# Optimization experiments

Measured on AMD Instinct MI355X. Metric: run time of the kernel, lower is better.

The kernel has to match this reference:

```python
import jax, jax.numpy as jnp
import numpy as np

N = 262144
FEAT = 64
D = 128
DEPTH = 2
N_LAYERS = 1
SCALE_FEATURES = 0.5
SCALE_STEPS = (1.0 - SCALE_FEATURES) / DEPTH
LN_EPS = 1e-5
SLOPE = 0.01


def leaky(x):
    return jnp.where(x >= 0, x, SLOPE * x)


def layernorm(x):
    mu = x.mean(-1, keepdims=True)
    var = ((x - mu) ** 2).mean(-1, keepdims=True)
    return (x - mu) / jnp.sqrt(var + LN_EPS)


def setup_inputs() -> dict:
    key = jax.random.key(0)
    ks = jax.random.split(key, 12)
    raw_feats = jax.random.normal(ks[0], (N, FEAT), dtype=jnp.float32)
    uids = jnp.arange(N, dtype=jnp.int32)
    id_map = jax.random.randint(ks[1], (N, 1, 2), 0, N, dtype=jnp.int32)
    # FeatureEmbedder params
    slow_mean = jnp.zeros((FEAT,), jnp.float32)
    slow_std = jnp.ones((FEAT,), jnp.float32)
    W_embd = jax.random.normal(ks[2], (FEAT, D), jnp.float32) / np.sqrt(FEAT)
    b_embd = jnp.zeros((D,), jnp.float32)
    Wl = jax.random.normal(ks[3], (N_LAYERS, D, D), jnp.float32) / np.sqrt(D)
    bl = jnp.zeros((N_LAYERS, D), jnp.float32)
    # node_emb params
    W_node = jax.random.normal(ks[4], (D, D), jnp.float32) / np.sqrt(D)
    b_node = jnp.zeros((D,), jnp.float32)
    rezero = jnp.full((1,), 0.1, jnp.float32)  # nonzero so depth loop is active
    W_w = jax.random.normal(ks[5], (D, 1), jnp.float32) * 0.01
    W_v = jax.random.normal(ks[6], (D, 1), jnp.float32) / np.sqrt(D)
    return {
        'raw_feats': raw_feats, 'uids': uids, 'id_map': id_map,
        'slow_mean': slow_mean, 'slow_std': slow_std,
        'W_embd': W_embd, 'b_embd': b_embd, 'Wl': Wl, 'bl': bl,
        'W_node': W_node, 'b_node': b_node, 'rezero': rezero,
        'W_w': W_w, 'W_v': W_v,
    }


def reference(raw_feats, uids, id_map, slow_mean, slow_std, W_embd, b_embd,
              Wl, bl, W_node, b_node, rezero, W_w, W_v):
    # sorted_feats = cat([raw_feats, zeros(1, FEAT)])  -> [N+1, FEAT]
    sorted_feats = jnp.concatenate(
        [raw_feats, jnp.zeros((1, FEAT), raw_feats.dtype)], axis=0)

    # FeatureEmbedder: SlowNorm -> Linear -> leaky, residual blocks, LayerNorm, *scale
    x = (sorted_feats - slow_mean) / (slow_std + 0.001)
    x = leaky(x @ W_embd + b_embd)
    for i in range(N_LAYERS):
        # F.leaky_relu(Sequential(Linear, LeakyReLU)(x)) + x  (double leaky)
        x = leaky(leaky(x @ Wl[i] + bl[i])) + x
    x = layernorm(x) * SCALE_FEATURES  # [N+1, D]

    # uids == arange(N), so uid-value -> row-index lookup is identity
    ids = id_map[:, 0, :]  # [N, 2] row indices into x

    for _ in range(DEPTH):
        feats = x[ids].mean(axis=1)                 # gather [N,2,D] -> mean -> [N,D]
        feats = leaky(feats @ W_node + b_node)       # node_emb
        new = x[:-1] + feats * (SCALE_STEPS * rezero)
        x = jnp.concatenate([new, x[-1:]], axis=0)   # scatter-update rows [:-1]

    x_main = x[:-1]
    w = x_main @ W_w                                  # weight head, no bias
    v = jax.lax.stop_gradient(x_main) @ W_v           # value head on detached x
    return (x_main, w, v)
```

## Files before the change

### kernel.cpp

```cpp
#include <hip/hip_runtime.h>


#define NROWS 262144
#define NBLK  4096

typedef __attribute__((ext_vector_type(8))) short bhalf8;
typedef __attribute__((ext_vector_type(4))) float f32x4;
typedef __attribute__((ext_vector_type(4))) unsigned int u32x4;

__device__ __forceinline__ unsigned short f2bf(float x) {
    union { float f; unsigned u; } v; v.f = x;
    unsigned r = v.u + 0x7FFFu + ((v.u >> 16) & 1u);
    return (unsigned short)(r >> 16);
}
__device__ __forceinline__ float bflo(unsigned u) {
    union { unsigned u; float f; } v; v.u = u << 16; return v.f;
}
__device__ __forceinline__ float bfhi(unsigned u) {
    union { unsigned u; float f; } v; v.u = u & 0xFFFF0000u; return v.f;
}
__device__ __forceinline__ float leaky(float x) { return x >= 0.0f ? x : 0.01f * x; }

__global__ void __launch_bounds__(256)
setup_kernel(const float* __restrict__ smean, const float* __restrict__ sstd,
             const float* __restrict__ Wemb, const float* __restrict__ bemb,
             const float* __restrict__ Wl, const float* __restrict__ Wn,
             unsigned short* __restrict__ wpack, float* __restrict__ bembP)
{
    int task = blockIdx.x * 256 + threadIdx.x;
    if (blockIdx.x < 160) {
        if (task < 8192) {
            int f = task >> 9, idx = task & 511;
            int t = f >> 1, s = f & 1, lane = idx >> 3, j = idx & 7;
            int n = t * 16 + (lane & 15), k = s * 32 + (lane >> 4) * 8 + j;
            wpack[task] = f2bf(Wemb[k * 128 + n] / (sstd[k] + 0.001f));
        } else if (task < 24576) {
            int u = task - 8192;
            int f = u >> 9, idx = u & 511;
            int t = f >> 2, s = f & 3, lane = idx >> 3, j = idx & 7;
            int n = t * 16 + (lane & 15), k = s * 32 + (lane >> 4) * 8 + j;
            wpack[task] = f2bf(Wl[k * 128 + n]);
        } else if (task < 40960) {
            int u = task - 24576;
            int f = u >> 9, idx = u & 511;
            int t = f >> 2, s = f & 3, lane = idx >> 3, j = idx & 7;
            int n = t * 16 + (lane & 15), k = s * 32 + (lane >> 4) * 8 + j;
            wpack[task] = f2bf(0.5f * Wn[k * 128 + n]);
        }
    } else {
        int n = threadIdx.x;
        if (n < 128) {
            float acc = bemb[n];
            for (int k = 0; k < 64; k++)
                acc -= smean[k] / (sstd[k] + 0.001f) * Wemb[k * 128 + n];
            bembP[n] = acc;
        }
    }
}

__global__ void __launch_bounds__(256)
phase_a_kernel(const float* __restrict__ feats,
               const unsigned short* __restrict__ wembF,
               const float* __restrict__ bembP,
               const unsigned short* __restrict__ wlF,
               const float* __restrict__ bl,
               unsigned short* __restrict__ xout)
{
    __shared__ __align__(16) short hb[64 * 136];
    const int tid = threadIdx.x, lane = tid & 63, wv = tid >> 6;
    const int m = lane & 15, q = lane >> 4;
    const int r0 = blockIdx.x * 64;

    const bhalf8* wbe = (const bhalf8*)wembF;
    const bhalf8* wbl = (const bhalf8*)wlF;

    bhalf8 af[2];
    #pragma unroll
    for (int s = 0; s < 2; s++) {
        const float* fp = feats + (size_t)(r0 + wv * 16 + m) * 64 + s * 32 + q * 8;
        f32x4 f0 = *(const f32x4*)fp;
        f32x4 f1 = *(const f32x4*)(fp + 4);
        bhalf8 a;
        #pragma unroll
        for (int jj = 0; jj < 4; jj++) { a[jj] = (short)f2bf(f0[jj]); a[4 + jj] = (short)f2bf(f1[jj]); }
        af[s] = a;
    }
    f32x4 acc[8] = {};
    #pragma unroll
    for (int s = 0; s < 2; s++)
        #pragma unroll
        for (int t = 0; t < 8; t++)
            acc[t] = __builtin_amdgcn_mfma_f32_16x16x32_bf16(af[s], wbe[(t * 2 + s) * 64 + lane], acc[t], 0, 0, 0);

    float hv[8][4];
    #pragma unroll
    for (int t = 0; t < 8; t++) {
        float be = bembP[t * 16 + m];
        #pragma unroll
        for (int p = 0; p < 4; p++) {
            float h = leaky(acc[t][p] + be);
            hv[t][p] = h;
            hb[(wv * 16 + q * 4 + p) * 136 + t * 16 + m] = (short)f2bf(h);
        }
    }
    f32x4 acc2[8] = {};
    #pragma unroll
    for (int s = 0; s < 4; s++) {
        bhalf8 a = *(const bhalf8*)&hb[(wv * 16 + m) * 136 + s * 32 + q * 8];
        #pragma unroll
        for (int t = 0; t < 8; t++)
            acc2[t] = __builtin_amdgcn_mfma_f32_16x16x32_bf16(a, wbl[(t * 4 + s) * 64 + lane], acc2[t], 0, 0, 0);
    }

    float tv[8][4];
    float sum[4] = {0, 0, 0, 0}, ssq[4] = {0, 0, 0, 0};
    #pragma unroll
    for (int t = 0; t < 8; t++) {
        float bb = bl[t * 16 + m];
        #pragma unroll
        for (int p = 0; p < 4; p++) {
            float v = leaky(leaky(acc2[t][p] + bb)) + hv[t][p];
            tv[t][p] = v;
            sum[p] += v; ssq[p] += v * v;
        }
    }
    #pragma unroll
    for (int p = 0; p < 4; p++) {
        #pragma unroll
        for (int d = 1; d < 16; d <<= 1) {
            sum[p] += __shfl_xor(sum[p], d, 64);
            ssq[p] += __shfl_xor(ssq[p], d, 64);
        }
    }
    #pragma unroll
    for (int p = 0; p < 4; p++) {
        float mu  = sum[p] * (1.0f / 128.0f);
        float var = ssq[p] * (1.0f / 128.0f) - mu * mu;
        float rs  = rsqrtf(var + 1e-5f) * 0.5f;
        int row = wv * 16 + q * 4 + p;
        #pragma unroll
        for (int t = 0; t < 8; t++)
            hb[row * 136 + t * 16 + m] = (short)f2bf((tv[t][p] - mu) * rs);
    }
    __syncthreads();
    for (int c = tid; c < 64 * 16; c += 256) {
        int row = c >> 4, cb = (c & 15) * 8;
        *reinterpret_cast<u32x4*>(&xout[(size_t)(r0 + row) * 128 + cb]) =
            *reinterpret_cast<const u32x4*>(&hb[row * 136 + cb]);
    }
}

template <typename TOUT>
__global__ void __launch_bounds__(256)
prop_kernel(const unsigned short* __restrict__ xin, const int* __restrict__ idmap,
            const unsigned short* __restrict__ wnF, const float* __restrict__ bn,
            const float* __restrict__ rez, const float* __restrict__ Ww,
            const float* __restrict__ Wv, TOUT* __restrict__ xout,
            float* __restrict__ wout, float* __restrict__ vout, int final_pass)
{
    __shared__ __align__(16) short gls[64 * 136];
    const int tid = threadIdx.x, lane = tid & 63, wv = tid >> 6;
    const int m = lane & 15, q = lane >> 4;
    const int r0 = blockIdx.x * 64;
    const bhalf8* wbn = (const bhalf8*)wnF;

    const int myrow = r0 + wv * 16 + m;
    int2 ids = ((const int2*)idmap)[myrow];
    const unsigned short* xa = xin + (size_t)ids.x * 128;
    const unsigned short* xb = xin + (size_t)ids.y * 128;
    bhalf8 afr[4];
    #pragma unroll
    for (int s = 0; s < 4; s++) {
        u32x4 ua = *(const u32x4*)(xa + s * 32 + q * 8);
        u32x4 ub = *(const u32x4*)(xb + s * 32 + q * 8);
        bhalf8 o;
        #pragma unroll
        for (int w = 0; w < 4; w++) {
            float lo = bflo(ua[w]) + bflo(ub[w]);
            float hi = bfhi(ua[w]) + bfhi(ub[w]);
            o[2 * w]     = (short)f2bf(lo);
            o[2 * w + 1] = (short)f2bf(hi);
        }
        afr[s] = o;
    }

    f32x4 acc[8] = {};
    #pragma unroll
    for (int s = 0; s < 4; s++)
        #pragma unroll
        for (int t = 0; t < 8; t++)
            acc[t] = __builtin_amdgcn_mfma_f32_16x16x32_bf16(afr[s], wbn[(t * 4 + s) * 64 + lane], acc[t], 0, 0, 0);

    const float scale = 0.25f * rez[0];
    #pragma unroll
    for (int t = 0; t < 8; t++) {
        float bb = bn[t * 16 + m];
        #pragma unroll
        for (int p = 0; p < 4; p++)
            gls[(wv * 16 + q * 4 + p) * 136 + t * 16 + m] = (short)f2bf(leaky(acc[t][p] + bb) * scale);
    }
    __syncthreads();

    #pragma unroll
    for (int i = 0; i < 4; i++) {
        int task = i * 256 + tid;
        int row = task >> 4, cb = task & 15;
        u32x4 gv = *(const u32x4*)&gls[row * 136 + cb * 8];
        u32x4 xv = *(const u32x4*)(xin + (size_t)(r0 + row) * 128 + cb * 8);
        float xn[8];
        #pragma unroll
        for (int w = 0; w < 4; w++) {
            xn[2 * w]     = bflo(xv[w]) + bflo(gv[w]);
            xn[2 * w + 1] = bfhi(xv[w]) + bfhi(gv[w]);
        }
        if (!final_pass) {
            u32x4 ov;
            #pragma unroll
            for (int w = 0; w < 4; w++)
                ov[w] = (unsigned)f2bf(xn[2 * w]) | ((unsigned)f2bf(xn[2 * w + 1]) << 16);
            *reinterpret_cast<u32x4*>(reinterpret_cast<unsigned short*>(xout) + (size_t)(r0 + row) * 128 + cb * 8) = ov;
        } else {
            float* op = reinterpret_cast<float*>(xout) + (size_t)(r0 + row) * 128 + cb * 8;
            f32x4 o0, o1;
            #pragma unroll
            for (int w = 0; w < 4; w++) { o0[w] = xn[w]; o1[w] = xn[4 + w]; }
            *reinterpret_cast<f32x4*>(op)     = o0;
            *reinterpret_cast<f32x4*>(op + 4) = o1;
            f32x4 w0 = *(const f32x4*)&Ww[cb * 8], w1 = *(const f32x4*)&Ww[cb * 8 + 4];
            f32x4 v0 = *(const f32x4*)&Wv[cb * 8], v1 = *(const f32x4*)&Wv[cb * 8 + 4];
            float ws = 0.0f, vs = 0.0f;
            #pragma unroll
            for (int w = 0; w < 4; w++) {
                ws += xn[w] * w0[w] + xn[4 + w] * w1[w];
                vs += xn[w] * v0[w] + xn[4 + w] * v1[w];
            }
            #pragma unroll
            for (int d = 1; d < 16; d <<= 1) {
                ws += __shfl_xor(ws, d, 64);
                vs += __shfl_xor(vs, d, 64);
            }
            if ((lane & 15) == 0) { wout[r0 + row] = ws; vout[r0 + row] = vs; }
        }
    }
}

extern "C" void kernel_launch(void* const* d_in, const int* in_sizes, int n_in,
                              void* d_out, int out_size, void* d_ws, size_t ws_size,
                              hipStream_t stream) {
    const float* feats = (const float*)d_in[0];
    const int*   idmap = (const int*)d_in[2];
    const float* smean = (const float*)d_in[3];
    const float* sstd  = (const float*)d_in[4];
    const float* Wemb  = (const float*)d_in[5];
    const float* bemb  = (const float*)d_in[6];
    const float* Wl    = (const float*)d_in[7];
    const float* bl    = (const float*)d_in[8];
    const float* Wn    = (const float*)d_in[9];
    const float* bn    = (const float*)d_in[10];
    const float* rez   = (const float*)d_in[11];
    const float* Ww    = (const float*)d_in[12];
    const float* Wv    = (const float*)d_in[13];

    char* ws = (char*)d_ws;
    unsigned short* wpack = (unsigned short*)ws;
    float*          bembP = (float*)(ws + 81920);
    unsigned short* x1    = (unsigned short*)(ws + (1 << 20));

    float* out = (float*)d_out;
    unsigned short* x0 = (unsigned short*)d_out;
    float* wout = out + (size_t)NROWS * 128;
    float* vout = wout + NROWS;

    setup_kernel<<<161, 256, 0, stream>>>(smean, sstd, Wemb, bemb, Wl, Wn, wpack, bembP);
    phase_a_kernel<<<NBLK, 256, 0, stream>>>(feats, wpack, bembP, wpack + 8192, bl, x0);
    prop_kernel<unsigned short><<<NBLK, 256, 0, stream>>>(x0, idmap, wpack + 24576, bn, rez, Ww, Wv,
                                                          x1, nullptr, nullptr, 0);
    prop_kernel<float><<<NBLK, 256, 0, stream>>>(x1, idmap, wpack + 24576, bn, rez, Ww, Wv,
                                                 out, wout, vout, 1);
}
```

Before: 344.8 us.

## Gather neighbor rows from an fp8 shadow copy to halve random-gather traffic

Phase A and the first propagation pass now also write an fp8 copy of x, laid out so each lane's K-slices sit contiguously. The propagation kernels gather the two neighbor rows from this fp8 copy instead of the bf16 copy, cutting the bytes of the random gather in half. The kernel also prefetches its own x rows into registers early and adds occupancy hints to the launch bounds. The cost is extra fp8 writes and a precision loss on the gathered features, which could break tolerance.

```diff
diff --git a/kernel.cpp b/kernel.cpp
--- a/kernel.cpp
+++ b/kernel.cpp
@@ -6,7 +6,9 @@
 
 typedef __attribute__((ext_vector_type(8))) short bhalf8;
 typedef __attribute__((ext_vector_type(4))) float f32x4;
+typedef __attribute__((ext_vector_type(2))) float f32x2;
 typedef __attribute__((ext_vector_type(4))) unsigned int u32x4;
+typedef __attribute__((ext_vector_type(2))) unsigned int u32x2;
 
 __device__ __forceinline__ unsigned short f2bf(float x) {
     union { float f; unsigned u; } v; v.f = x;
@@ -20,6 +22,12 @@
     union { unsigned u; float f; } v; v.u = u & 0xFFFF0000u; return v.f;
 }
 __device__ __forceinline__ float leaky(float x) { return x >= 0.0f ? x : 0.01f * x; }
+
+__device__ __forceinline__ unsigned pk4fp8(float a, float b, float c, float d) {
+    int r = __builtin_amdgcn_cvt_pk_fp8_f32(a, b, 0, false);
+    r = __builtin_amdgcn_cvt_pk_fp8_f32(c, d, r, true);
+    return (unsigned)r;
+}
 
 __global__ void __launch_bounds__(256)
 setup_kernel(const float* __restrict__ smean, const float* __restrict__ sstd,
@@ -58,13 +66,14 @@
     }
 }
 
-__global__ void __launch_bounds__(256)
+__global__ void __launch_bounds__(256, 4)
 phase_a_kernel(const float* __restrict__ feats,
                const unsigned short* __restrict__ wembF,
                const float* __restrict__ bembP,
                const unsigned short* __restrict__ wlF,
                const float* __restrict__ bl,
-               unsigned short* __restrict__ xout)
+               unsigned short* __restrict__ xout,
+               unsigned char* __restrict__ xf8)
 {
     __shared__ __align__(16) short hb[64 * 136];
     const int tid = threadIdx.x, lane = tid & 63, wv = tid >> 6;
@@ -92,16 +101,19 @@
         for (int t = 0; t < 8; t++)
             acc[t] = __builtin_amdgcn_mfma_f32_16x16x32_bf16(af[s], wbe[(t * 2 + s) * 64 + lane], acc[t], 0, 0, 0);
 
-    float hv[8][4];
+    unsigned hvp[8][2];
     #pragma unroll
     for (int t = 0; t < 8; t++) {
         float be = bembP[t * 16 + m];
+        unsigned short hq[4];
         #pragma unroll
         for (int p = 0; p < 4; p++) {
             float h = leaky(acc[t][p] + be);
-            hv[t][p] = h;
-            hb[(wv * 16 + q * 4 + p) * 136 + t * 16 + m] = (short)f2bf(h);
-        }
+            hq[p] = f2bf(h);
+            hb[(wv * 16 + q * 4 + p) * 136 + t * 16 + m] = (short)hq[p];
+        }
+        hvp[t][0] = (unsigned)hq[0] | ((unsigned)hq[1] << 16);
+        hvp[t][1] = (unsigned)hq[2] | ((unsigned)hq[3] << 16);
     }
     f32x4 acc2[8] = {};
     #pragma unroll
@@ -117,9 +129,12 @@
     #pragma unroll
     for (int t = 0; t < 8; t++) {
         float bb = bl[t * 16 + m];
+        float h0 = bflo(hvp[t][0]), h1 = bfhi(hvp[t][0]);
+        float h2 = bflo(hvp[t][1]), h3 = bfhi(hvp[t][1]);
+        float hvv[4] = { h0, h1, h2, h3 };
         #pragma unroll
         for (int p = 0; p < 4; p++) {
-            float v = leaky(leaky(acc2[t][p] + bb)) + hv[t][p];
+            float v = leaky(leaky(acc2[t][p] + bb)) + hvv[p];
             tv[t][p] = v;
             sum[p] += v; ssq[p] += v * v;
         }
@@ -144,18 +159,25 @@
     }
     __syncthreads();
     for (int c = tid; c < 64 * 16; c += 256) {
-        int row = c >> 4, cb = (c & 15) * 8;
-        *reinterpret_cast<u32x4*>(&xout[(size_t)(r0 + row) * 128 + cb]) =
-            *reinterpret_cast<const u32x4*>(&hb[row * 136 + cb]);
+        int row = c >> 4, cb = c & 15;
+        u32x4 hv4 = *reinterpret_cast<const u32x4*>(&hb[row * 136 + cb * 8]);
+        *reinterpret_cast<u32x4*>(&xout[(size_t)(r0 + row) * 128 + cb * 8]) = hv4;
+        u32x2 pf;
+        pf[0] = pk4fp8(bflo(hv4[0]), bfhi(hv4[0]), bflo(hv4[1]), bfhi(hv4[1]));
+        pf[1] = pk4fp8(bflo(hv4[2]), bfhi(hv4[2]), bflo(hv4[3]), bfhi(hv4[3]));
+        *reinterpret_cast<u32x2*>(xf8 + (size_t)(r0 + row) * 128 + (cb & 3) * 32 + (cb >> 2) * 8) = pf;
     }
 }
 
 template <typename TOUT>
-__global__ void __launch_bounds__(256)
-prop_kernel(const unsigned short* __restrict__ xin, const int* __restrict__ idmap,
+__global__ void __launch_bounds__(256, 5)
+prop_kernel(const unsigned short* __restrict__ xin,
+            const unsigned char* __restrict__ xf8,
+            const int* __restrict__ idmap,
             const unsigned short* __restrict__ wnF, const float* __restrict__ bn,
             const float* __restrict__ rez, const float* __restrict__ Ww,
             const float* __restrict__ Wv, TOUT* __restrict__ xout,
+            unsigned char* __restrict__ xf8out,
             float* __restrict__ wout, float* __restrict__ vout, int final_pass)
 {
     __shared__ __align__(16) short gls[64 * 136];
@@ -164,23 +186,41 @@
     const int r0 = blockIdx.x * 64;
     const bhalf8* wbn = (const bhalf8*)wnF;
 
+    const int crow = tid >> 4, ccb = tid & 15;
+    u32x4 xown[4];
+    #pragma unroll
+    for (int i = 0; i < 4; i++)
+        xown[i] = *reinterpret_cast<const u32x4*>(xin + (size_t)(r0 + i * 16 + crow) * 128 + ccb * 8);
+
     const int myrow = r0 + wv * 16 + m;
     int2 ids = ((const int2*)idmap)[myrow];
-    const unsigned short* xa = xin + (size_t)ids.x * 128;
-    const unsigned short* xb = xin + (size_t)ids.y * 128;
+    const unsigned char* pa = xf8 + (size_t)ids.x * 128 + q * 32;
+    const unsigned char* pb = xf8 + (size_t)ids.y * 128 + q * 32;
+    u32x4 ga0 = *(const u32x4*)pa;
+    u32x4 ga1 = *(const u32x4*)(pa + 16);
+    u32x4 gb0 = *(const u32x4*)pb;
+    u32x4 gb1 = *(const u32x4*)(pb + 16);
+
     bhalf8 afr[4];
     #pragma unroll
     for (int s = 0; s < 4; s++) {
-        u32x4 ua = *(const u32x4*)(xa + s * 32 + q * 8);
-        u32x4 ub = *(const u32x4*)(xb + s * 32 + q * 8);
+        unsigned a0 = (s < 2) ? ga0[(s & 1) * 2]     : ga1[(s & 1) * 2];
+        unsigned a1 = (s < 2) ? ga0[(s & 1) * 2 + 1] : ga1[(s & 1) * 2 + 1];
+        unsigned b0 = (s < 2) ? gb0[(s & 1) * 2]     : gb1[(s & 1) * 2];
+        unsigned b1 = (s < 2) ? gb0[(s & 1) * 2 + 1] : gb1[(s & 1) * 2 + 1];
+        f32x2 s01 = __builtin_amdgcn_cvt_pk_f32_fp8((int)a0, false);
+        f32x2 s23 = __builtin_amdgcn_cvt_pk_f32_fp8((int)a0, true);
+        f32x2 s45 = __builtin_amdgcn_cvt_pk_f32_fp8((int)a1, false);
+        f32x2 s67 = __builtin_amdgcn_cvt_pk_f32_fp8((int)a1, true);
+        f32x2 t01 = __builtin_amdgcn_cvt_pk_f32_fp8((int)b0, false);
+        f32x2 t23 = __builtin_amdgcn_cvt_pk_f32_fp8((int)b0, true);
+        f32x2 t45 = __builtin_amdgcn_cvt_pk_f32_fp8((int)b1, false);
+        f32x2 t67 = __builtin_amdgcn_cvt_pk_f32_fp8((int)b1, true);
         bhalf8 o;
-        #pragma unroll
-        for (int w = 0; w < 4; w++) {
-            float lo = bflo(ua[w]) + bflo(ub[w]);
-            float hi = bfhi(ua[w]) + bfhi(ub[w]);
-            o[2 * w]     = (short)f2bf(lo);
-            o[2 * w + 1] = (short)f2bf(hi);
-        }
+        o[0] = (short)f2bf(s01[0] + t01[0]); o[1] = (short)f2bf(s01[1] + t01[1]);
+        o[2] = (short)f2bf(s23[0] + t23[0]); o[3] = (short)f2bf(s23[1] + t23[1]);
+        o[4] = (short)f2bf(s45[0] + t45[0]); o[5] = (short)f2bf(s45[1] + t45[1]);
+        o[6] = (short)f2bf(s67[0] + t67[0]); o[7] = (short)f2bf(s67[1] + t67[1]);
         afr[s] = o;
     }
 
@@ -203,10 +243,9 @@
 
     #pragma unroll
     for (int i = 0; i < 4; i++) {
-        int task = i * 256 + tid;
-        int row = task >> 4, cb = task & 15;
+        int row = i * 16 + crow, cb = ccb;
         u32x4 gv = *(const u32x4*)&gls[row * 136 + cb * 8];
-        u32x4 xv = *(const u32x4*)(xin + (size_t)(r0 + row) * 128 + cb * 8);
+        u32x4 xv = xown[i];
         float xn[8];
         #pragma unroll
         for (int w = 0; w < 4; w++) {
@@ -219,6 +258,10 @@
             for (int w = 0; w < 4; w++)
                 ov[w] = (unsigned)f2bf(xn[2 * w]) | ((unsigned)f2bf(xn[2 * w + 1]) << 16);
             *reinterpret_cast<u32x4*>(reinterpret_cast<unsigned short*>(xout) + (size_t)(r0 + row) * 128 + cb * 8) = ov;
+            u32x2 pf;
+            pf[0] = pk4fp8(xn[0], xn[1], xn[2], xn[3]);
+            pf[1] = pk4fp8(xn[4], xn[5], xn[6], xn[7]);
+            *reinterpret_cast<u32x2*>(xf8out + (size_t)(r0 + row) * 128 + (cb & 3) * 32 + (cb >> 2) * 8) = pf;
         } else {
             float* op = reinterpret_cast<float*>(xout) + (size_t)(r0 + row) * 128 + cb * 8;
             f32x4 o0, o1;
@@ -264,7 +307,9 @@
     char* ws = (char*)d_ws;
     unsigned short* wpack = (unsigned short*)ws;
     float*          bembP = (float*)(ws + 81920);
-    unsigned short* x1    = (unsigned short*)(ws + (1 << 20));
+    unsigned short* x1    = (unsigned short*)(ws + (1ull << 20));
+    unsigned char*  x0f8  = (unsigned char*)(ws + (65ull << 20));
+    unsigned char*  x1f8  = (unsigned char*)(ws + (97ull << 20));
 
     float* out = (float*)d_out;
     unsigned short* x0 = (unsigned short*)d_out;
@@ -272,9 +317,9 @@
     float* vout = wout + NROWS;
 
     setup_kernel<<<161, 256, 0, stream>>>(smean, sstd, Wemb, bemb, Wl, Wn, wpack, bembP);
-    phase_a_kernel<<<NBLK, 256, 0, stream>>>(feats, wpack, bembP, wpack + 8192, bl, x0);
-    prop_kernel<unsigned short><<<NBLK, 256, 0, stream>>>(x0, idmap, wpack + 24576, bn, rez, Ww, Wv,
-                                                          x1, nullptr, nullptr, 0);
-    prop_kernel<float><<<NBLK, 256, 0, stream>>>(x1, idmap, wpack + 24576, bn, rez, Ww, Wv,
-                                                 out, wout, vout, 1);
-}
+    phase_a_kernel<<<NBLK, 256, 0, stream>>>(feats, wpack, bembP, wpack + 8192, bl, x0, x0f8);
+    prop_kernel<unsigned short><<<NBLK, 256, 0, stream>>>(x0, x0f8, idmap, wpack + 24576, bn, rez, Ww, Wv,
+                                                          x1, x1f8, nullptr, nullptr, 0);
+    prop_kernel<float><<<NBLK, 256, 0, stream>>>(x1, x1f8, idmap, wpack + 24576, bn, rez, Ww, Wv,
+                                                 out, nullptr, wout, vout, 1);
+}
```

Measured after the change: 344.3 us. No clear change (-0.2%).

## Make phase_a and prop kernels persistent with register prefetch of next tile

Applied to the files above, without the earlier changes.

Shrinks the grid from 4096 to 1024 blocks; each block now loops over four 64-row tiles and prefetches the next tile's features, id pairs, gathered rows and own rows into registers while the current tile computes. Shared buffers are double-buffered per iteration, and phase_a rereads the residual from LDS instead of keeping it in registers. The aim is to hide gather and load latency behind MFMA work. The cost is more register pressure (launch bounds now request occupancy) and fewer blocks in flight to hide latency.

```diff
diff --git a/kernel.cpp b/kernel.cpp
--- a/kernel.cpp
+++ b/kernel.cpp
@@ -2,7 +2,8 @@
 
 
 #define NROWS 262144
-#define NBLK  4096
+#define NTILES 4096
+#define GRID  1024
 
 typedef __attribute__((ext_vector_type(8))) short bhalf8;
 typedef __attribute__((ext_vector_type(4))) float f32x4;
@@ -18,6 +19,9 @@
 }
 __device__ __forceinline__ float bfhi(unsigned u) {
     union { unsigned u; float f; } v; v.u = u & 0xFFFF0000u; return v.f;
+}
+__device__ __forceinline__ float bf2f(unsigned short s) {
+    union { unsigned u; float f; } v; v.u = ((unsigned)s) << 16; return v.f;
 }
 __device__ __forceinline__ float leaky(float x) { return x >= 0.0f ? x : 0.01f * x; }
 
@@ -58,7 +62,7 @@
     }
 }
 
-__global__ void __launch_bounds__(256)
+__global__ void __launch_bounds__(256, 4)
 phase_a_kernel(const float* __restrict__ feats,
                const unsigned short* __restrict__ wembF,
                const float* __restrict__ bembP,
@@ -66,180 +70,238 @@
                const float* __restrict__ bl,
                unsigned short* __restrict__ xout)
 {
-    __shared__ __align__(16) short hb[64 * 136];
+    __shared__ __align__(16) short hb[2][64 * 136];
     const int tid = threadIdx.x, lane = tid & 63, wv = tid >> 6;
     const int m = lane & 15, q = lane >> 4;
-    const int r0 = blockIdx.x * 64;
+    const int crow = tid >> 4, ccb = tid & 15;
 
     const bhalf8* wbe = (const bhalf8*)wembF;
     const bhalf8* wbl = (const bhalf8*)wlF;
 
-    bhalf8 af[2];
+    f32x4 fr[4], nfr[4];
+    {
+        const float* base = feats + (size_t)(blockIdx.x * 64 + wv * 16 + m) * 64 + q * 8;
+        #pragma unroll
+        for (int s = 0; s < 2; s++) {
+            fr[2 * s]     = *(const f32x4*)(base + s * 32);
+            fr[2 * s + 1] = *(const f32x4*)(base + s * 32 + 4);
+        }
+    }
+
     #pragma unroll
-    for (int s = 0; s < 2; s++) {
-        const float* fp = feats + (size_t)(r0 + wv * 16 + m) * 64 + s * 32 + q * 8;
-        f32x4 f0 = *(const f32x4*)fp;
-        f32x4 f1 = *(const f32x4*)(fp + 4);
-        bhalf8 a;
-        #pragma unroll
-        for (int jj = 0; jj < 4; jj++) { a[jj] = (short)f2bf(f0[jj]); a[4 + jj] = (short)f2bf(f1[jj]); }
-        af[s] = a;
-    }
-    f32x4 acc[8] = {};
-    #pragma unroll
-    for (int s = 0; s < 2; s++)
-        #pragma unroll
-        for (int t = 0; t < 8; t++)
-            acc[t] = __builtin_amdgcn_mfma_f32_16x16x32_bf16(af[s], wbe[(t * 2 + s) * 64 + lane], acc[t], 0, 0, 0);
-
-    float hv[8][4];
-    #pragma unroll
-    for (int t = 0; t < 8; t++) {
-        float be = bembP[t * 16 + m];
+    for (int it = 0; it < 4; ++it) {
+        const int r0 = (blockIdx.x + it * GRID) * 64;
+        if (it < 3) {
+            const float* base = feats + (size_t)(r0 + GRID * 64 + wv * 16 + m) * 64 + q * 8;
+            #pragma unroll
+            for (int s = 0; s < 2; s++) {
+                nfr[2 * s]     = *(const f32x4*)(base + s * 32);
+                nfr[2 * s + 1] = *(const f32x4*)(base + s * 32 + 4);
+            }
+        }
+        short* hbb = hb[it & 1];
+
+        bhalf8 af[2];
+        #pragma unroll
+        for (int s = 0; s < 2; s++) {
+            bhalf8 a;
+            #pragma unroll
+            for (int jj = 0; jj < 4; jj++) {
+                a[jj]     = (short)f2bf(fr[2 * s][jj]);
+                a[4 + jj] = (short)f2bf(fr[2 * s + 1][jj]);
+            }
+            af[s] = a;
+        }
+        f32x4 acc[8] = {};
+        #pragma unroll
+        for (int s = 0; s < 2; s++)
+            #pragma unroll
+            for (int t = 0; t < 8; t++)
+                acc[t] = __builtin_amdgcn_mfma_f32_16x16x32_bf16(af[s], wbe[(t * 2 + s) * 64 + lane], acc[t], 0, 0, 0);
+
+        #pragma unroll
+        for (int t = 0; t < 8; t++) {
+            float be = bembP[t * 16 + m];
+            #pragma unroll
+            for (int p = 0; p < 4; p++)
+                hbb[(wv * 16 + q * 4 + p) * 136 + t * 16 + m] = (short)f2bf(leaky(acc[t][p] + be));
+        }
+        f32x4 acc2[8] = {};
+        #pragma unroll
+        for (int s = 0; s < 4; s++) {
+            bhalf8 a = *(const bhalf8*)&hbb[(wv * 16 + m) * 136 + s * 32 + q * 8];
+            #pragma unroll
+            for (int t = 0; t < 8; t++)
+                acc2[t] = __builtin_amdgcn_mfma_f32_16x16x32_bf16(a, wbl[(t * 4 + s) * 64 + lane], acc2[t], 0, 0, 0);
+        }
+
+        float sum[4] = {0, 0, 0, 0}, ssq[4] = {0, 0, 0, 0};
+        #pragma unroll
+        for (int t = 0; t < 8; t++) {
+            float bb = bl[t * 16 + m];
+            #pragma unroll
+            for (int p = 0; p < 4; p++) {
+                float h = bf2f((unsigned short)hbb[(wv * 16 + q * 4 + p) * 136 + t * 16 + m]);
+                float v = leaky(leaky(acc2[t][p] + bb)) + h;
+                acc2[t][p] = v;
+                sum[p] += v; ssq[p] += v * v;
+            }
+        }
         #pragma unroll
         for (int p = 0; p < 4; p++) {
-            float h = leaky(acc[t][p] + be);
-            hv[t][p] = h;
-            hb[(wv * 16 + q * 4 + p) * 136 + t * 16 + m] = (short)f2bf(h);
-        }
-    }
-    f32x4 acc2[8] = {};
-    #pragma unroll
-    for (int s = 0; s < 4; s++) {
-        bhalf8 a = *(const bhalf8*)&hb[(wv * 16 + m) * 136 + s * 32 + q * 8];
-        #pragma unroll
-        for (int t = 0; t < 8; t++)
-            acc2[t] = __builtin_amdgcn_mfma_f32_16x16x32_bf16(a, wbl[(t * 4 + s) * 64 + lane], acc2[t], 0, 0, 0);
-    }
-
-    float tv[8][4];
-    float sum[4] = {0, 0, 0, 0}, ssq[4] = {0, 0, 0, 0};
-    #pragma unroll
-    for (int t = 0; t < 8; t++) {
-        float bb = bl[t * 16 + m];
+            #pragma unroll
+            for (int d = 1; d < 16; d <<= 1) {
+                sum[p] += __shfl_xor(sum[p], d, 64);
+                ssq[p] += __shfl_xor(ssq[p], d, 64);
+            }
+        }
         #pragma unroll
         for (int p = 0; p < 4; p++) {
-            float v = leaky(leaky(acc2[t][p] + bb)) + hv[t][p];
-            tv[t][p] = v;
-            sum[p] += v; ssq[p] += v * v;
-        }
-    }
-    #pragma unroll
-    for (int p = 0; p < 4; p++) {
-        #pragma unroll
-        for (int d = 1; d < 16; d <<= 1) {
-            sum[p] += __shfl_xor(sum[p], d, 64);
-            ssq[p] += __shfl_xor(ssq[p], d, 64);
-        }
-    }
-    #pragma unroll
-    for (int p = 0; p < 4; p++) {
-        float mu  = sum[p] * (1.0f / 128.0f);
-        float var = ssq[p] * (1.0f / 128.0f) - mu * mu;
-        float rs  = rsqrtf(var + 1e-5f) * 0.5f;
-        int row = wv * 16 + q * 4 + p;
-        #pragma unroll
-        for (int t = 0; t < 8; t++)
-            hb[row * 136 + t * 16 + m] = (short)f2bf((tv[t][p] - mu) * rs);
-    }
-    __syncthreads();
-    for (int c = tid; c < 64 * 16; c += 256) {
-        int row = c >> 4, cb = (c & 15) * 8;
-        *reinterpret_cast<u32x4*>(&xout[(size_t)(r0 + row) * 128 + cb]) =
-            *reinterpret_cast<const u32x4*>(&hb[row * 136 + cb]);
+            float mu  = sum[p] * (1.0f / 128.0f);
+            float var = ssq[p] * (1.0f / 128.0f) - mu * mu;
+            float rs  = rsqrtf(var + 1e-5f) * 0.5f;
+            int row = wv * 16 + q * 4 + p;
+            #pragma unroll
+            for (int t = 0; t < 8; t++)
+                hbb[row * 136 + t * 16 + m] = (short)f2bf((acc2[t][p] - mu) * rs);
+        }
+        __syncthreads();
+        #pragma unroll
+        for (int i = 0; i < 4; i++) {
+            int row = i * 16 + crow;
+            *reinterpret_cast<u32x4*>(&xout[(size_t)(r0 + row) * 128 + ccb * 8]) =
+                *reinterpret_cast<const u32x4*>(&hbb[row * 136 + ccb * 8]);
+        }
+        if (it < 3) {
+            #pragma unroll
+            for (int s = 0; s < 4; s++) fr[s] = nfr[s];
+        }
     }
 }
 
 template <typename TOUT>
-__global__ void __launch_bounds__(256)
+__global__ void __launch_bounds__(256, 3)
 prop_kernel(const unsigned short* __restrict__ xin, const int* __restrict__ idmap,
             const unsigned short* __restrict__ wnF, const float* __restrict__ bn,
             const float* __restrict__ rez, const float* __restrict__ Ww,
             const float* __restrict__ Wv, TOUT* __restrict__ xout,
             float* __restrict__ wout, float* __restrict__ vout, int final_pass)
 {
-    __shared__ __align__(16) short gls[64 * 136];
+    __shared__ __align__(16) short gls[2][64 * 136];
     const int tid = threadIdx.x, lane = tid & 63, wv = tid >> 6;
     const int m = lane & 15, q = lane >> 4;
-    const int r0 = blockIdx.x * 64;
+    const int crow = tid >> 4, ccb = tid & 15;
     const bhalf8* wbn = (const bhalf8*)wnF;
-
-    const int myrow = r0 + wv * 16 + m;
-    int2 ids = ((const int2*)idmap)[myrow];
-    const unsigned short* xa = xin + (size_t)ids.x * 128;
-    const unsigned short* xb = xin + (size_t)ids.y * 128;
-    bhalf8 afr[4];
+    const float scale = 0.25f * rez[0];
+
+    u32x4 ga[4], gb[4], xown[4];
+    u32x4 nga[4], ngb[4], nxown[4];
+
+    {
+        const int r0 = blockIdx.x * 64;
+        int2 ids = ((const int2*)idmap)[r0 + wv * 16 + m];
+        #pragma unroll
+        for (int i = 0; i < 4; i++)
+            xown[i] = *(const u32x4*)(xin + (size_t)(r0 + i * 16 + crow) * 128 + ccb * 8);
+        const unsigned short* xa = xin + (size_t)ids.x * 128 + q * 8;
+        const unsigned short* xb = xin + (size_t)ids.y * 128 + q * 8;
+        #pragma unroll
+        for (int s = 0; s < 4; s++) {
+            ga[s] = *(const u32x4*)(xa + s * 32);
+            gb[s] = *(const u32x4*)(xb + s * 32);
+        }
+    }
+
     #pragma unroll
-    for (int s = 0; s < 4; s++) {
-        u32x4 ua = *(const u32x4*)(xa + s * 32 + q * 8);
-        u32x4 ub = *(const u32x4*)(xb + s * 32 + q * 8);
-        bhalf8 o;
-        #pragma unroll
-        for (int w = 0; w < 4; w++) {
-            float lo = bflo(ua[w]) + bflo(ub[w]);
-            float hi = bfhi(ua[w]) + bfhi(ub[w]);
-            o[2 * w]     = (short)f2bf(lo);
-            o[2 * w + 1] = (short)f2bf(hi);
-        }
-        afr[s] = o;
-    }
-
-    f32x4 acc[8] = {};
-    #pragma unroll
-    for (int s = 0; s < 4; s++)
-        #pragma unroll
-        for (int t = 0; t < 8; t++)
-            acc[t] = __builtin_amdgcn_mfma_f32_16x16x32_bf16(afr[s], wbn[(t * 4 + s) * 64 + lane], acc[t], 0, 0, 0);
-
-    const float scale = 0.25f * rez[0];
-    #pragma unroll
-    for (int t = 0; t < 8; t++) {
-        float bb = bn[t * 16 + m];
-        #pragma unroll
-        for (int p = 0; p < 4; p++)
-            gls[(wv * 16 + q * 4 + p) * 136 + t * 16 + m] = (short)f2bf(leaky(acc[t][p] + bb) * scale);
-    }
-    __syncthreads();
-
-    #pragma unroll
-    for (int i = 0; i < 4; i++) {
-        int task = i * 256 + tid;
-        int row = task >> 4, cb = task & 15;
-        u32x4 gv = *(const u32x4*)&gls[row * 136 + cb * 8];
-        u32x4 xv = *(const u32x4*)(xin + (size_t)(r0 + row) * 128 + cb * 8);
-        float xn[8];
-        #pragma unroll
-        for (int w = 0; w < 4; w++) {
-            xn[2 * w]     = bflo(xv[w]) + bflo(gv[w]);
-            xn[2 * w + 1] = bfhi(xv[w]) + bfhi(gv[w]);
-        }
-        if (!final_pass) {
-            u32x4 ov;
-            #pragma unroll
-            for (int w = 0; w < 4; w++)
-                ov[w] = (unsigned)f2bf(xn[2 * w]) | ((unsigned)f2bf(xn[2 * w + 1]) << 16);
-            *reinterpret_cast<u32x4*>(reinterpret_cast<unsigned short*>(xout) + (size_t)(r0 + row) * 128 + cb * 8) = ov;
-        } else {
-            float* op = reinterpret_cast<float*>(xout) + (size_t)(r0 + row) * 128 + cb * 8;
-            f32x4 o0, o1;
-            #pragma unroll
-            for (int w = 0; w < 4; w++) { o0[w] = xn[w]; o1[w] = xn[4 + w]; }
-            *reinterpret_cast<f32x4*>(op)     = o0;
-            *reinterpret_cast<f32x4*>(op + 4) = o1;
-            f32x4 w0 = *(const f32x4*)&Ww[cb * 8], w1 = *(const f32x4*)&Ww[cb * 8 + 4];
-            f32x4 v0 = *(const f32x4*)&Wv[cb * 8], v1 = *(const f32x4*)&Wv[cb * 8 + 4];
-            float ws = 0.0f, vs = 0.0f;
+    for (int it = 0; it < 4; ++it) {
+        const int r0 = (blockIdx.x + it * GRID) * 64;
+        int2 nids;
+        if (it < 3) {
+            nids = ((const int2*)idmap)[r0 + GRID * 64 + wv * 16 + m];
+            #pragma unroll
+            for (int i = 0; i < 4; i++)
+                nxown[i] = *(const u32x4*)(xin + (size_t)(r0 + GRID * 64 + i * 16 + crow) * 128 + ccb * 8);
+        }
+
+        f32x4 acc[8] = {};
+        #pragma unroll
+        for (int s = 0; s < 4; s++) {
+            bhalf8 a;
             #pragma unroll
             for (int w = 0; w < 4; w++) {
-                ws += xn[w] * w0[w] + xn[4 + w] * w1[w];
-                vs += xn[w] * v0[w] + xn[4 + w] * v1[w];
-            }
-            #pragma unroll
-            for (int d = 1; d < 16; d <<= 1) {
-                ws += __shfl_xor(ws, d, 64);
-                vs += __shfl_xor(vs, d, 64);
-            }
-            if ((lane & 15) == 0) { wout[r0 + row] = ws; vout[r0 + row] = vs; }
+                a[2 * w]     = (short)f2bf(bflo(ga[s][w]) + bflo(gb[s][w]));
+                a[2 * w + 1] = (short)f2bf(bfhi(ga[s][w]) + bfhi(gb[s][w]));
+            }
+            #pragma unroll
+            for (int t = 0; t < 8; t++)
+                acc[t] = __builtin_amdgcn_mfma_f32_16x16x32_bf16(a, wbn[(t * 4 + s) * 64 + lane], acc[t], 0, 0, 0);
+        }
+
+        if (it < 3) {
+            const unsigned short* xa = xin + (size_t)nids.x * 128 + q * 8;
+            const unsigned short* xb = xin + (size_t)nids.y * 128 + q * 8;
+            #pragma unroll
+            for (int s = 0; s < 4; s++) {
+                nga[s] = *(const u32x4*)(xa + s * 32);
+                ngb[s] = *(const u32x4*)(xb + s * 32);
+            }
+        }
+
+        short* g = gls[it & 1];
+        #pragma unroll
+        for (int t = 0; t < 8; t++) {
+            float bb = bn[t * 16 + m];
+            #pragma unroll
+            for (int p = 0; p < 4; p++)
+                g[(wv * 16 + q * 4 + p) * 136 + t * 16 + m] = (short)f2bf(leaky(acc[t][p] + bb) * scale);
+        }
+        __syncthreads();
+
+        #pragma unroll
+        for (int i = 0; i < 4; i++) {
+            int row = i * 16 + crow;
+            u32x4 gv = *(const u32x4*)&g[row * 136 + ccb * 8];
+            u32x4 xv = xown[i];
+            float xn[8];
+            #pragma unroll
+            for (int w = 0; w < 4; w++) {
+                xn[2 * w]     = bflo(xv[w]) + bflo(gv[w]);
+                xn[2 * w + 1] = bfhi(xv[w]) + bfhi(gv[w]);
+            }
+            if (!final_pass) {
+                u32x4 ov;
+                #pragma unroll
+                for (int w = 0; w < 4; w++)
+                    ov[w] = (unsigned)f2bf(xn[2 * w]) | ((unsigned)f2bf(xn[2 * w + 1]) << 16);
+                *reinterpret_cast<u32x4*>(reinterpret_cast<unsigned short*>(xout) + (size_t)(r0 + row) * 128 + ccb * 8) = ov;
+            } else {
+                float* op = reinterpret_cast<float*>(xout) + (size_t)(r0 + row) * 128 + ccb * 8;
+                f32x4 o0, o1;
+                #pragma unroll
+                for (int w = 0; w < 4; w++) { o0[w] = xn[w]; o1[w] = xn[4 + w]; }
+                *reinterpret_cast<f32x4*>(op)     = o0;
+                *reinterpret_cast<f32x4*>(op + 4) = o1;
+                f32x4 w0 = *(const f32x4*)&Ww[ccb * 8], w1 = *(const f32x4*)&Ww[ccb * 8 + 4];
+                f32x4 v0 = *(const f32x4*)&Wv[ccb * 8], v1 = *(const f32x4*)&Wv[ccb * 8 + 4];
+                float ws = 0.0f, vs = 0.0f;
+                #pragma unroll
+                for (int w = 0; w < 4; w++) {
+                    ws += xn[w] * w0[w] + xn[4 + w] * w1[w];
+                    vs += xn[w] * v0[w] + xn[4 + w] * v1[w];
+                }
+                #pragma unroll
+                for (int d = 1; d < 16; d <<= 1) {
+                    ws += __shfl_xor(ws, d, 64);
+                    vs += __shfl_xor(vs, d, 64);
+                }
+                if ((lane & 15) == 0) { wout[r0 + row] = ws; vout[r0 + row] = vs; }
+            }
+        }
+        if (it < 3) {
+            #pragma unroll
+            for (int s = 0; s < 4; s++) { ga[s] = nga[s]; gb[s] = ngb[s]; }
+            #pragma unroll
+            for (int i = 0; i < 4; i++) xown[i] = nxown[i];
         }
     }
 }
@@ -264,7 +326,7 @@
     char* ws = (char*)d_ws;
     unsigned short* wpack = (unsigned short*)ws;
     float*          bembP = (float*)(ws + 81920);
-    unsigned short* x1    = (unsigned short*)(ws + (1 << 20));
+    unsigned short* x1    = (unsigned short*)(ws + (1ull << 20));
 
     float* out = (float*)d_out;
     unsigned short* x0 = (unsigned short*)d_out;
@@ -272,9 +334,9 @@
     float* vout = wout + NROWS;
 
     setup_kernel<<<161, 256, 0, stream>>>(smean, sstd, Wemb, bemb, Wl, Wn, wpack, bembP);
-    phase_a_kernel<<<NBLK, 256, 0, stream>>>(feats, wpack, bembP, wpack + 8192, bl, x0);
-    prop_kernel<unsigned short><<<NBLK, 256, 0, stream>>>(x0, idmap, wpack + 24576, bn, rez, Ww, Wv,
+    phase_a_kernel<<<GRID, 256, 0, stream>>>(feats, wpack, bembP, wpack + 8192, bl, x0);
+    prop_kernel<unsigned short><<<GRID, 256, 0, stream>>>(x0, idmap, wpack + 24576, bn, rez, Ww, Wv,
                                                           x1, nullptr, nullptr, 0);
-    prop_kernel<float><<<NBLK, 256, 0, stream>>>(x1, idmap, wpack + 24576, bn, rez, Ww, Wv,
+    prop_kernel<float><<<GRID, 256, 0, stream>>>(x1, idmap, wpack + 24576, bn, rez, Ww, Wv,
                                                  out, wout, vout, 1);
 }
```

After: 440.7 us. +27.8%, slower.
